# Kernel optimization log

Measured on AMD Instinct MI355X. Metric: run time of the kernel, lower is better.

## Reference

```python
import jax, jax.numpy as jnp
import numpy as np

N_NODES = 100000
N_EDGES = 1600000
HIDDEN = 128
N_GRAPHS = 64
N_CLASSES = 10


def setup_inputs() -> dict:
    key = jax.random.key(0)
    ks = jax.random.split(key, 10)
    x = jax.random.normal(ks[0], (N_NODES, 1), dtype=jnp.float32)
    edge_index = jax.random.randint(ks[1], (2, N_EDGES), 0, N_NODES, dtype=jnp.int32)
    batch = jnp.sort(jax.random.randint(ks[2], (N_NODES,), 0, N_GRAPHS, dtype=jnp.int32))
    def glorot(k, shape):
        fan_in, fan_out = shape
        s = jnp.sqrt(6.0 / (fan_in + fan_out))
        return jax.random.uniform(k, shape, jnp.float32, -s, s)
    return {
        "x": x,
        "edge_index": edge_index,
        "batch": batch,
        "W1l": glorot(ks[3], (1, HIDDEN)),
        "W1r": glorot(ks[4], (1, HIDDEN)),
        "b1": jnp.zeros((HIDDEN,), jnp.float32),
        "W2l": glorot(ks[5], (HIDDEN, HIDDEN)),
        "W2r": glorot(ks[6], (HIDDEN, HIDDEN)),
        "b2": jnp.zeros((HIDDEN,), jnp.float32),
        "W3l": glorot(ks[7], (HIDDEN, HIDDEN)),
        "W3r": glorot(ks[8], (HIDDEN, HIDDEN)),
        "b3": jnp.zeros((HIDDEN,), jnp.float32),
        "Wfc": glorot(ks[9], (HIDDEN, N_CLASSES)),
        "bfc": jnp.zeros((N_CLASSES,), jnp.float32),
    }


def _sage_conv(x, src, dst, Wl, Wr, b, n_nodes):
    # mean aggregation of source features at destination nodes
    msg = x[src]                                              # [E, d_in]
    agg = jax.ops.segment_sum(msg, dst, num_segments=n_nodes)  # [N, d_in]
    cnt = jax.ops.segment_sum(jnp.ones((src.shape[0], 1), x.dtype), dst,
                              num_segments=n_nodes)            # [N, 1]
    mean = agg / jnp.maximum(cnt, 1.0)
    # PyG SAGEConv: lin_l(mean neighbors) + bias + lin_r(self)
    return mean @ Wl + b + x @ Wr


def reference(x, edge_index, batch, W1l, W1r, b1, W2l, W2r, b2,
              W3l, W3r, b3, Wfc, bfc):
    src, dst = edge_index[0], edge_index[1]
    n = x.shape[0]
    h = jax.nn.relu(_sage_conv(x, src, dst, W1l, W1r, b1, n))
    h = jax.nn.relu(_sage_conv(h, src, dst, W2l, W2r, b2, n))
    h = jax.nn.relu(_sage_conv(h, src, dst, W3l, W3r, b3, n))
    # global_mean_pool over graph ids in `batch`
    pooled = jax.ops.segment_sum(h, batch, num_segments=N_GRAPHS)
    gcnt = jax.ops.segment_sum(jnp.ones((n, 1), h.dtype), batch,
                               num_segments=N_GRAPHS)
    pooled = pooled / jnp.maximum(gcnt, 1.0)
    logits = pooled @ Wfc + bfc
    return jax.nn.log_softmax(logits, axis=1)
```

## Files before the change

### kernel.cpp

```cpp
#include <hip/hip_runtime.h>

typedef unsigned int u32;
typedef unsigned short u16;
typedef short bf16x8 __attribute__((ext_vector_type(8)));
typedef float f32x4 __attribute__((ext_vector_type(4)));
typedef float f32x2 __attribute__((ext_vector_type(2)));
typedef u32 u32x4 __attribute__((ext_vector_type(4)));

#define HBLK 256
#define PCAP 2560

__device__ __forceinline__ u16 f2bf(float f) {
  u32 u = __float_as_uint(f);
  u = (u + 0x7FFFu + ((u >> 16) & 1u)) >> 16;
  return (u16)u;
}
__device__ __forceinline__ float bf2f(u32 h) { return __uint_as_float(h << 16); }

__global__ void hist_wprep_kernel(const int* __restrict__ dst, int* __restrict__ boff,
                                  int* __restrict__ btotal, int E, int nbuk, int chunk,
                                  const float* __restrict__ W2l, const float* __restrict__ W2r,
                                  const float* __restrict__ W3l, const float* __restrict__ W3r,
                                  u16* __restrict__ wt2, u16* __restrict__ wt3,
                                  const int* __restrict__ batch, int* __restrict__ gcnt, int n) {
  int tid = threadIdx.x;
  int idx = blockIdx.x * 1024 + tid;
  if (idx < 65536) {
    int which = idx >> 15, r = idx & 32767;
    int j = r >> 8, k = r & 255;
    if (which == 0) {
      float v = (k < 128) ? W2l[k * 128 + j] : W2r[(k - 128) * 128 + j];
      wt2[r] = f2bf(v);
    } else {
      float v = (k < 128) ? W3l[k * 128 + j] : W3r[(k - 128) * 128 + j];
      wt3[r] = f2bf(v);
    }
  }
  __shared__ int h[1024];
  __shared__ int gh[64];
  for (int i = tid; i < nbuk; i += 1024) h[i] = 0;
  if (tid < 64) gh[tid] = 0;
  __syncthreads();
  int b0 = blockIdx.x * chunk, b1 = min(b0 + chunk, E);
  int len = max(b1 - b0, 0);
  int ng = len >> 2;
  for (int g4 = tid; g4 < ng; g4 += 1024) {
    u32x4 d4 = *(const u32x4*)(dst + b0 + g4 * 4);
#pragma unroll
    for (int w = 0; w < 4; ++w) atomicAdd(&h[(int)d4[w] >> 7], 1);
  }
  for (int e = b0 + ng * 4 + tid; e < b1; e += 1024)
    atomicAdd(&h[dst[e] >> 7], 1);
  int chunkN = (n + HBLK - 1) / HBLK;
  int n0 = blockIdx.x * chunkN, n1 = min(n0 + chunkN, n);
  for (int i = n0 + tid; i < n1; i += 1024)
    atomicAdd(&gh[batch[i]], 1);
  __syncthreads();
  for (int i = tid; i < nbuk; i += 1024)
    boff[blockIdx.x * 1024 + i] = atomicAdd(&btotal[i], h[i]);
  if (tid < 64 && gh[tid] > 0)
    atomicAdd(&gcnt[tid], gh[tid]);
}

__global__ void scatter2_kernel(const int* __restrict__ src, const int* __restrict__ dst,
                                const int* __restrict__ btotal, const int* __restrict__ boff,
                                u32* __restrict__ part, int* __restrict__ bbase,
                                int E, int nbuk, int chunk) {
  __shared__ int wsum[1024];
  __shared__ int cur[1024];
  int tid = threadIdx.x;
  int v = (tid < nbuk) ? btotal[tid] : 0;
  wsum[tid] = v;
  __syncthreads();
  for (int off = 1; off < 1024; off <<= 1) {
    int t = (tid >= off) ? wsum[tid - off] : 0;
    __syncthreads();
    wsum[tid] += t;
    __syncthreads();
  }
  int excl = wsum[tid] - v;
  if (tid < nbuk) {
    cur[tid] = excl + boff[blockIdx.x * 1024 + tid];
    if (blockIdx.x == 0) bbase[tid] = excl;
  }
  __syncthreads();
  int b0 = blockIdx.x * chunk, b1 = min(b0 + chunk, E);
  int len = max(b1 - b0, 0);
  int ng = len >> 2;
  for (int g4 = tid; g4 < ng; g4 += 1024) {
    int e = b0 + g4 * 4;
    u32x4 s4 = *(const u32x4*)(src + e);
    u32x4 d4 = *(const u32x4*)(dst + e);
#pragma unroll
    for (int w = 0; w < 4; ++w) {
      int d = (int)d4[w];
      int pos = atomicAdd(&cur[d >> 7], 1);
      part[pos] = s4[w] | ((u32)(d & 127) << 25);
    }
  }
  for (int e = b0 + ng * 4 + tid; e < b1; e += 1024) {
    int d = dst[e];
    int pos = atomicAdd(&cur[d >> 7], 1);
    part[pos] = (u32)src[e] | ((u32)(d & 127) << 25);
  }
}

__global__ void scatter3_kernel(const u32* __restrict__ part, const int* __restrict__ bbase,
                                const float* __restrict__ x,
                                const float* __restrict__ W1l, const float* __restrict__ W1r,
                                const float* __restrict__ b1,
                                int* __restrict__ roff, int* __restrict__ csr,
                                u32* __restrict__ h1, int E, int nbuk, int n) {
  int b = blockIdx.x;
  int tid = threadIdx.x;
  int base = bbase[b];
  int end = (b + 1 < nbuk) ? bbase[b + 1] : E;
  int len = end - base;
  int cap = min(len, PCAP);
  __shared__ u32 plds[PCAP];
  __shared__ int cnt[128];
  __shared__ int s[128];
  __shared__ int cur[128];
  __shared__ float xsum[128];
  __shared__ float meanv[128];
  __shared__ float wlA[128], wrA[128], bA[128];
  if (tid < 128) {
    cnt[tid] = 0; xsum[tid] = 0.f;
    wlA[tid] = W1l[tid]; wrA[tid] = W1r[tid]; bA[tid] = b1[tid];
  }
  for (int e = tid; e < cap; e += 512) plds[e] = part[base + e];
  __syncthreads();
  for (int e = tid; e < len; e += 512) {
    u32 p = (e < cap) ? plds[e] : part[base + e];
    atomicAdd(&cnt[p >> 25], 1);
  }
  __syncthreads();
  if (tid < 128) s[tid] = cnt[tid];
  __syncthreads();
  for (int off = 1; off < 128; off <<= 1) {
    int t = (tid >= off && tid < 128) ? s[tid - off] : 0;
    __syncthreads();
    if (tid < 128) s[tid] += t;
    __syncthreads();
  }
  if (tid < 128) {
    int excl = s[tid] - cnt[tid];
    cur[tid] = base + excl;
    int node = b * 128 + tid;
    if (node < n) roff[node] = base + excl;
  }
  if (b == 0 && tid == 0) roff[n] = E;
  __syncthreads();
  for (int e = tid; e < len; e += 512) {
    u32 p = (e < cap) ? plds[e] : part[base + e];
    int sidx = (int)(p & 0x1FFFFFFu);
    int pos = atomicAdd(&cur[p >> 25], 1);
    csr[pos] = sidx;
    atomicAdd(&xsum[p >> 25], x[sidx]);
  }
  __syncthreads();
  if (tid < 128) meanv[tid] = xsum[tid] / (float)max(cnt[tid], 1);
  __syncthreads();
  int nlocal = min(128, n - b * 128);
  for (int q = tid; q < nlocal * 64; q += 512) {
    int ln = q >> 6, w = q & 63;
    int node = b * 128 + ln;
    int j0 = w * 2;
    float m = meanv[ln], xs = x[node];
    float v0 = fmaxf(m * wlA[j0] + xs * wrA[j0] + bA[j0], 0.f);
    float v1 = fmaxf(m * wlA[j0 + 1] + xs * wrA[j0 + 1] + bA[j0 + 1], 0.f);
    h1[(size_t)node * 64 + w] = (u32)f2bf(v0) | ((u32)f2bf(v1) << 16);
  }
}

__device__ __forceinline__ u32x4 grow(const u32* hp, int s) {
  return *(const u32x4*)(hp + (size_t)s * 64);
}
__device__ __forceinline__ void acc_row(f32x2* a, u32x4 v) {
#pragma unroll
  for (int w = 0; w < 4; ++w)
    a[w] += (f32x2){bf2f(v[w] & 0xFFFFu), bf2f(v[w] >> 16)};
}

__global__ void agg_kernel(const int* __restrict__ csr, const int* __restrict__ roff,
                           const u32* __restrict__ hin, u32* __restrict__ outv, int n) {
  int g = threadIdx.x >> 4, li = threadIdx.x & 15;
  int i = blockIdx.x * 16 + g;
  if (i >= n) return;
  int e0 = roff[i], e1 = roff[i + 1];
  f32x2 a[4] = {};
  const u32* hp = hin + li * 4;
  int e = e0;
  for (; e + 7 < e1; e += 8) {
    int s0 = csr[e], s1 = csr[e + 1], s2 = csr[e + 2], s3 = csr[e + 3];
    int s4 = csr[e + 4], s5 = csr[e + 5], s6 = csr[e + 6], s7 = csr[e + 7];
    u32x4 v0 = grow(hp, s0), v1 = grow(hp, s1), v2 = grow(hp, s2), v3 = grow(hp, s3);
    u32x4 v4 = grow(hp, s4), v5 = grow(hp, s5), v6 = grow(hp, s6), v7 = grow(hp, s7);
    acc_row(a, v0); acc_row(a, v1); acc_row(a, v2); acc_row(a, v3);
    acc_row(a, v4); acc_row(a, v5); acc_row(a, v6); acc_row(a, v7);
  }
  for (; e + 3 < e1; e += 4) {
    int s0 = csr[e], s1 = csr[e + 1], s2 = csr[e + 2], s3 = csr[e + 3];
    u32x4 v0 = grow(hp, s0), v1 = grow(hp, s1), v2 = grow(hp, s2), v3 = grow(hp, s3);
    acc_row(a, v0); acc_row(a, v1); acc_row(a, v2); acc_row(a, v3);
  }
  for (; e < e1; ++e) acc_row(a, grow(hp, csr[e]));
  float inv = 1.f / (float)max(e1 - e0, 1);
  u32x4 o;
#pragma unroll
  for (int w = 0; w < 4; ++w)
    o[w] = (u32)f2bf(a[w].x * inv) | ((u32)f2bf(a[w].y * inv) << 16);
  *(u32x4*)(outv + (size_t)i * 64 + li * 4) = o;
}

template <int MODE>
__launch_bounds__(512)
__global__ void mm_kernel(const u16* Aleft, const u16* Aright,
                          const u16* __restrict__ Wt, const float* __restrict__ bias,
                          u16* Out, const int* __restrict__ batch,
                          float* __restrict__ pooled, int n) {
  __shared__ u16 wlds[32768];
  __shared__ int bgp[128];
  for (int c = threadIdx.x; c < 4096; c += 512) {
    int j = c >> 5, ch = c & 31;
    int swz = ch ^ (j & 31);
    *(u32x4*)(&wlds[j * 256 + swz * 8]) = *(const u32x4*)(&Wt[j * 256 + ch * 8]);
  }
  __syncthreads();
  int wave = threadIdx.x >> 6;
  int lane = threadIdx.x & 63;
  int quad = lane >> 4, l16 = lane & 15;
  int row0 = blockIdx.x * 128 + wave * 16;
  int m = row0 + l16;
  int mc = m < n ? m : (n - 1);
  f32x4 acc[8] = {};
  const u16* Ah[2] = {Aleft, Aright};
#pragma unroll
  for (int half = 0; half < 2; ++half) {
    const u16* A = Ah[half] + (size_t)mc * 128;
#pragma unroll
    for (int s = 0; s < 4; ++s) {
      bf16x8 a = *(const bf16x8*)(A + s * 32 + quad * 8);
      int chunk = (half << 4) + (s << 2) + quad;
#pragma unroll
      for (int t = 0; t < 8; ++t) {
        int j = t * 16 + l16;
        int swz = chunk ^ (j & 31);
        bf16x8 b = *(const bf16x8*)(&wlds[j * 256 + swz * 8]);
        acc[t] = __builtin_amdgcn_mfma_f32_16x16x32_bf16(a, b, acc[t], 0, 0, 0);
      }
    }
  }
  __syncthreads();
  int rl_base = wave * 16 + quad * 4;
#pragma unroll
  for (int t = 0; t < 8; ++t) {
    int j = t * 16 + l16;
    float bj = bias[j];
#pragma unroll
    for (int r = 0; r < 4; ++r) {
      float v = acc[t][r] + bj;
      wlds[(rl_base + r) * 136 + j] = f2bf(fmaxf(v, 0.f));
    }
  }
  if (MODE == 1) {
    if (threadIdx.x < 128) {
      int rr = blockIdx.x * 128 + threadIdx.x;
      bgp[threadIdx.x] = (rr < n) ? batch[rr] : -1;
    }
  }
  __syncthreads();
  if (MODE == 0) {
    int base_row = blockIdx.x * 128;
    for (int q = 0; q < 4; ++q) {
      int idx = q * 512 + threadIdx.x;
      int rl = idx >> 4;
      int ch = idx & 15;
      int mr = base_row + rl;
      if (mr < n)
        *(u32x4*)(&Out[(size_t)mr * 128 + ch * 8]) =
            *(const u32x4*)(&wlds[rl * 136 + ch * 8]);
    }
  } else {
    int tcol = threadIdx.x & 127, seg = threadIdx.x >> 7;
    float accp = 0.f;
    int gcur = -1;
    for (int r = seg * 32; r < seg * 32 + 32; ++r) {
      int gb = bgp[r];
      if (gb != gcur) {
        if (gcur >= 0) atomicAdd(&pooled[gcur * 128 + tcol], accp);
        gcur = gb;
        accp = 0.f;
      }
      if (gb >= 0) accp += bf2f((u32)wlds[r * 136 + tcol]);
    }
    if (gcur >= 0) atomicAdd(&pooled[gcur * 128 + tcol], accp);
  }
}

__global__ void head_kernel(const float* __restrict__ pooled, const int* __restrict__ gcnt,
                            const float* __restrict__ Wfc, const float* __restrict__ bfc,
                            float* __restrict__ out) {
  __shared__ float lg[64][10];
  int t = threadIdx.x;
  if (t < 640) {
    int g = t / 10, c = t % 10;
    float inv = 1.f / (float)max(gcnt[g], 1);
    float acc = bfc[c];
    for (int k = 0; k < 128; ++k) acc += pooled[g * 128 + k] * inv * Wfc[k * 10 + c];
    lg[g][c] = acc;
  }
  __syncthreads();
  if (t < 640) {
    int g = t / 10, c = t % 10;
    float mx = -1e30f;
    for (int q = 0; q < 10; ++q) mx = fmaxf(mx, lg[g][q]);
    float se = 0.f;
    for (int q = 0; q < 10; ++q) se += expf(lg[g][q] - mx);
    out[g * 10 + c] = lg[g][c] - mx - logf(se);
  }
}

extern "C" void kernel_launch(void* const* d_in, const int* in_sizes, int n_in,
                              void* d_out, int out_size, void* d_ws, size_t ws_size,
                              hipStream_t stream) {
  const float* x   = (const float*)d_in[0];
  const int* ei    = (const int*)d_in[1];
  const int* batch = (const int*)d_in[2];
  const float* W1l = (const float*)d_in[3];
  const float* W1r = (const float*)d_in[4];
  const float* b1  = (const float*)d_in[5];
  const float* W2l = (const float*)d_in[6];
  const float* W2r = (const float*)d_in[7];
  const float* b2  = (const float*)d_in[8];
  const float* W3l = (const float*)d_in[9];
  const float* W3r = (const float*)d_in[10];
  const float* b3  = (const float*)d_in[11];
  const float* Wfc = (const float*)d_in[12];
  const float* bfc = (const float*)d_in[13];
  float* out = (float*)d_out;
  int N = in_sizes[0];
  int E = in_sizes[1] / 2;
  const int* src = ei;
  const int* dst = ei + E;

  char* p = (char*)d_ws;
  auto alloc = [&](size_t bytes) { void* r = (void*)p; p += (bytes + 255) & ~(size_t)255; return r; };
  int* roff   = (int*)alloc((size_t)(N + 1) * 4);
  int* csr    = (int*)alloc((size_t)E * 4);
  u32* bufA   = (u32*)alloc((size_t)N * 64 * 4);
  u32* bufB   = (u32*)alloc((size_t)N * 64 * 4);
  u16* wt2    = (u16*)alloc(32768 * 2);
  u16* wt3    = (u16*)alloc(32768 * 2);
  float* pooled = (float*)alloc(64 * 128 * 4);
  int* gcnt   = (int*)alloc(64 * 4);
  int* btotal = (int*)alloc(1024 * 4);
  int* bbase  = (int*)alloc(1024 * 4);

  int nbuk = (N + 127) >> 7;
  int* boff = (int*)bufA;
  u32* part = (u32*)bufB;
  int chunk = (((E + HBLK - 1) / HBLK) + 3) & ~3;

  hipMemsetAsync(pooled, 0, 32768 + 256 + 4096, stream);
  hist_wprep_kernel<<<HBLK, 1024, 0, stream>>>(dst, boff, btotal, E, nbuk, chunk,
                                               W2l, W2r, W3l, W3r, wt2, wt3,
                                               batch, gcnt, N);
  scatter2_kernel<<<HBLK, 1024, 0, stream>>>(src, dst, btotal, boff, part, bbase,
                                             E, nbuk, chunk);
  scatter3_kernel<<<nbuk, 512, 0, stream>>>(part, bbase, x, W1l, W1r, b1,
                                            roff, csr, bufA, E, nbuk, N);
  agg_kernel<<<(N + 15) / 16, 256, 0, stream>>>(csr, roff, bufA, bufB, N);
  mm_kernel<0><<<(N + 127) / 128, 512, 0, stream>>>((const u16*)bufB, (const u16*)bufA,
                                                    wt2, b2, (u16*)bufB, batch, pooled, N);
  agg_kernel<<<(N + 15) / 16, 256, 0, stream>>>(csr, roff, bufB, bufA, N);
  mm_kernel<1><<<(N + 127) / 128, 512, 0, stream>>>((const u16*)bufA, (const u16*)bufB,
                                                    wt3, b3, (u16*)bufA, batch, pooled, N);
  head_kernel<<<1, 640, 0, stream>>>(pooled, gcnt, Wfc, bfc, out);
}
```

Before: 298.3 us.

## Fuse classifier head into final matmul via last-block counter; double histogram blocks

Removes the separate head kernel launch by having the last finishing block of the final mm_kernel compute the logits and log-softmax. It uses an atomic done counter zeroed by the existing memset. The histogram/scatter grid also grows from 256 to 512 blocks to spread the edge work. Block completion order now matters, and a single-block tail is added to the matmul.

```diff
diff --git a/kernel.cpp b/kernel.cpp
--- a/kernel.cpp
+++ b/kernel.cpp
@@ -7,7 +7,7 @@
 typedef float f32x2 __attribute__((ext_vector_type(2)));
 typedef u32 u32x4 __attribute__((ext_vector_type(4)));
 
-#define HBLK 256
+#define HBLK 512
 #define PCAP 2560
 
 __device__ __forceinline__ u16 f2bf(float f) {
@@ -218,8 +218,11 @@
 __global__ void mm_kernel(const u16* Aleft, const u16* Aright,
                           const u16* __restrict__ Wt, const float* __restrict__ bias,
                           u16* Out, const int* __restrict__ batch,
-                          float* __restrict__ pooled, int n) {
-  __shared__ u16 wlds[32768];
+                          float* __restrict__ pooled, int* __restrict__ done,
+                          const int* __restrict__ gcnt,
+                          const float* __restrict__ Wfc, const float* __restrict__ bfc,
+                          float* __restrict__ out, int n) {
+  __shared__ __align__(16) u16 wlds[32768];
   __shared__ int bgp[128];
   for (int c = threadIdx.x; c < 4096; c += 512) {
     int j = c >> 5, ch = c & 31;
@@ -295,29 +298,40 @@
       if (gb >= 0) accp += bf2f((u32)wlds[r * 136 + tcol]);
     }
     if (gcur >= 0) atomicAdd(&pooled[gcur * 128 + tcol], accp);
-  }
-}
-
-__global__ void head_kernel(const float* __restrict__ pooled, const int* __restrict__ gcnt,
-                            const float* __restrict__ Wfc, const float* __restrict__ bfc,
-                            float* __restrict__ out) {
-  __shared__ float lg[64][10];
-  int t = threadIdx.x;
-  if (t < 640) {
-    int g = t / 10, c = t % 10;
-    float inv = 1.f / (float)max(gcnt[g], 1);
-    float acc = bfc[c];
-    for (int k = 0; k < 128; ++k) acc += pooled[g * 128 + k] * inv * Wfc[k * 10 + c];
-    lg[g][c] = acc;
-  }
-  __syncthreads();
-  if (t < 640) {
-    int g = t / 10, c = t % 10;
-    float mx = -1e30f;
-    for (int q = 0; q < 10; ++q) mx = fmaxf(mx, lg[g][q]);
-    float se = 0.f;
-    for (int q = 0; q < 10; ++q) se += expf(lg[g][q] - mx);
-    out[g * 10 + c] = lg[g][c] - mx - logf(se);
+    __threadfence();
+    __shared__ int lastBlk;
+    if (threadIdx.x == 0) {
+      int t = atomicAdd(done, 1);
+      lastBlk = (t == (int)gridDim.x - 1) ? 1 : 0;
+    }
+    __syncthreads();
+    if (!lastBlk) return;
+    float* plds = (float*)wlds;
+    float* lg = plds + 8192;
+    __shared__ float ginv[64];
+    for (int i = threadIdx.x; i < 8192; i += 512)
+      plds[i] = __hip_atomic_load(&pooled[i], __ATOMIC_RELAXED, __HIP_MEMORY_SCOPE_AGENT);
+    if (threadIdx.x < 64) {
+      int gc = __hip_atomic_load(&gcnt[threadIdx.x], __ATOMIC_RELAXED, __HIP_MEMORY_SCOPE_AGENT);
+      ginv[threadIdx.x] = 1.f / (float)max(gc, 1);
+    }
+    __syncthreads();
+    for (int t = threadIdx.x; t < 640; t += 512) {
+      int g = t / 10, c = t % 10;
+      float acc2 = bfc[c];
+      float inv = ginv[g];
+      for (int k = 0; k < 128; ++k) acc2 += plds[g * 128 + k] * inv * Wfc[k * 10 + c];
+      lg[t] = acc2;
+    }
+    __syncthreads();
+    for (int t = threadIdx.x; t < 640; t += 512) {
+      int g = t / 10, c = t % 10;
+      float mx = -1e30f;
+      for (int q = 0; q < 10; ++q) mx = fmaxf(mx, lg[g * 10 + q]);
+      float se = 0.f;
+      for (int q = 0; q < 10; ++q) se += expf(lg[g * 10 + q] - mx);
+      out[g * 10 + c] = lg[g * 10 + c] - mx - logf(se);
+    }
   }
 }
 
@@ -355,6 +369,7 @@
   float* pooled = (float*)alloc(64 * 128 * 4);
   int* gcnt   = (int*)alloc(64 * 4);
   int* btotal = (int*)alloc(1024 * 4);
+  int* done   = (int*)alloc(256);
   int* bbase  = (int*)alloc(1024 * 4);
 
   int nbuk = (N + 127) >> 7;
@@ -362,7 +377,7 @@
   u32* part = (u32*)bufB;
   int chunk = (((E + HBLK - 1) / HBLK) + 3) & ~3;
 
-  hipMemsetAsync(pooled, 0, 32768 + 256 + 4096, stream);
+  hipMemsetAsync(pooled, 0, 32768 + 256 + 4096 + 256, stream);
   hist_wprep_kernel<<<HBLK, 1024, 0, stream>>>(dst, boff, btotal, E, nbuk, chunk,
                                                W2l, W2r, W3l, W3r, wt2, wt3,
                                                batch, gcnt, N);
@@ -372,9 +387,10 @@
                                             roff, csr, bufA, E, nbuk, N);
   agg_kernel<<<(N + 15) / 16, 256, 0, stream>>>(csr, roff, bufA, bufB, N);
   mm_kernel<0><<<(N + 127) / 128, 512, 0, stream>>>((const u16*)bufB, (const u16*)bufA,
-                                                    wt2, b2, (u16*)bufB, batch, pooled, N);
+                                                    wt2, b2, (u16*)bufB, batch, pooled,
+                                                    done, gcnt, Wfc, bfc, out, N);
   agg_kernel<<<(N + 15) / 16, 256, 0, stream>>>(csr, roff, bufB, bufA, N);
   mm_kernel<1><<<(N + 127) / 128, 512, 0, stream>>>((const u16*)bufA, (const u16*)bufB,
-                                                    wt3, b3, (u16*)bufA, batch, pooled, N);
-  head_kernel<<<1, 640, 0, stream>>>(pooled, gcnt, Wfc, bfc, out);
-}
+                                                    wt3, b3, (u16*)bufA, batch, pooled,
+                                                    done, gcnt, Wfc, bfc, out, N);
+}
```

After: 391.4 us. 1.31x slower.
